# Kernel tuning notes

Hardware: AMD Instinct MI355X
Metric: run time of the kernel (lower is better)

## Reference

```python
import jax, jax.numpy as jnp
import numpy as np

L, B, S, H = 2, 32, 2048, 256  # layers, batch, seqlen, hidden (=input_size)


def setup_inputs() -> dict:
    key = jax.random.key(0)
    k0, k1, k2, k3, k4 = jax.random.split(key, 5)
    scale = 1.0 / np.sqrt(H)
    inputs = jax.random.normal(k0, (B, S, H), jnp.float32)
    W_ih = jax.random.uniform(k1, (L, 4 * H, H), jnp.float32, -scale, scale)
    b_ih = jax.random.uniform(k2, (L, 4 * H), jnp.float32, -scale, scale)
    W_hh = jax.random.uniform(k3, (L, 4 * H, H), jnp.float32, -scale, scale)
    b_hh = jax.random.uniform(k4, (L, 4 * H), jnp.float32, -scale, scale)
    return {"inputs": inputs, "W_ih": W_ih, "b_ih": b_ih, "W_hh": W_hh, "b_hh": b_hh}


def _lstm_layer(x, Wi, bi, Wh, bh):
    # Precompute input projection for the whole sequence (matches cells[l].ih(prev_layer)).
    xp = jnp.einsum('bsh,gh->bsg', x, Wi) + bi  # [B, S, 4H]
    hid = Wh.shape[1]
    h0 = jnp.zeros((x.shape[0], hid), x.dtype)
    c0 = jnp.zeros((x.shape[0], hid), x.dtype)

    def step(carry, xt):
        h, c = carry
        gates = xt + h @ Wh.T + bh          # [B, 4H]
        i, f, g, o = jnp.split(gates, 4, axis=-1)
        c = jax.nn.sigmoid(f) * c + jax.nn.sigmoid(i) * jnp.tanh(g)
        h = jax.nn.sigmoid(o) * jnpp_tanh(c) if False else jax.nn.sigmoid(o) * jnp.tanh(c)
        return (h, c), h

    (hT, cT), ys = jax.lax.scan(step, (h0, c0), jnp.swapaxes(xp, 0, 1))  # scan over time
    return jnp.swapaxes(ys, 0, 1), hT, cT  # [B, S, H], [B, H], [B, H]


def reference(inputs, W_ih, b_ih, W_hh, b_hh):
    # Eval-mode forward: locked dropout is identity; hiddens initialized to zeros.
    x = inputs
    hs, cs = [], []
    for l in range(W_ih.shape[0]):
        x, hT, cT = _lstm_layer(x, W_ih[l], b_ih[l], W_hh[l], b_hh[l])
        hs.append(hT)
        cs.append(cT)
    # outputs [B,S,H]; final hiddens each [L,B,H]
    return x, jnp.stack(hs, axis=0), jnp.stack(cs, axis=0)
```

## Files before the change

### kernel.cpp

```cpp
#include <hip/hip_runtime.h>
#include <cstdint>
#include <cstddef>

typedef _Float16 half_t;
typedef _Float16 half2_t __attribute__((ext_vector_type(2)));
typedef _Float16 half8_t __attribute__((ext_vector_type(8)));
typedef float   float4_t __attribute__((ext_vector_type(4)));

#define L_N 2
#define B_N 32
#define S_N 2048
#define H_N 256
#define G_N 1024
#define M_N (B_N*S_N)

#define RING_R 4
#define RING_BYTES (B_N*RING_R*128*8)

#define WS_A0   0ull
#define WS_XP   33554432ull
#define WS_WI   167772160ull
#define WS_WH   168820736ull
#define WS_BSUM 169869312ull
#define WS_HP0  169877504ull
#define WS_HP1  170008576ull

__global__ void cvt_f32_f16(const float* __restrict__ in, half_t* __restrict__ out, int n){
  int i = blockIdx.x*256 + threadIdx.x;
  if (i < n) out[i] = (half_t)in[i];
}

__global__ void make_bsum(const float* __restrict__ bi, const float* __restrict__ bh,
                          float* __restrict__ bs, int n){
  int i = blockIdx.x*256 + threadIdx.x;
  if (i < n) bs[i] = bi[i] + bh[i];
}

__global__ __launch_bounds__(256) void gemm_xp(
    const half_t* __restrict__ A, const half_t* __restrict__ W,
    const float* __restrict__ bsum, half_t* __restrict__ XP)
{
  const int wave = threadIdx.x >> 6;
  const int lane = threadIdx.x & 63;
  const int l15 = lane & 15, quad = lane >> 4;
  const int m0 = blockIdx.x*64 + wave*16;
  const int n0 = blockIdx.y*64;
  float4_t acc[4] = {{0,0,0,0},{0,0,0,0},{0,0,0,0},{0,0,0,0}};
  const half_t* arow = A + (size_t)(m0 + l15)*H_N + quad*8;
  const half_t* brow[4];
  #pragma unroll
  for (int nt=0; nt<4; ++nt)
    brow[nt] = W + (size_t)(n0 + nt*16 + l15)*H_N + quad*8;
  #pragma unroll
  for (int k0=0; k0<H_N; k0+=32){
    half8_t af = *(const half8_t*)(arow + k0);
    #pragma unroll
    for (int nt=0; nt<4; ++nt){
      half8_t bf = *(const half8_t*)(brow[nt] + k0);
      acc[nt] = __builtin_amdgcn_mfma_f32_16x16x32_f16(af, bf, acc[nt], 0, 0, 0);
    }
  }
  #pragma unroll
  for (int nt=0; nt<4; ++nt){
    const int col = n0 + nt*16 + l15;
    const int cell = col & 255, gate = col >> 8;
    const float bs = bsum[col];
    #pragma unroll
    for (int r=0; r<4; ++r){
      XP[(size_t)(m0 + quad*4 + r)*G_N + cell*4 + gate] = (half_t)(acc[nt][r] + bs);
    }
  }
}

__device__ __forceinline__ float sigf(float x){ return 1.f/(1.f + __expf(-x)); }
__device__ __forceinline__ float tanh_f(float x){ return 1.f - 2.f/(__expf(2.f*x) + 1.f); }

__device__ __forceinline__ uint32_t ring_poll(const unsigned long long* p, unsigned tag){
  unsigned long long v;
  do { v = __hip_atomic_load(p, __ATOMIC_RELAXED, __HIP_MEMORY_SCOPE_AGENT); }
  while ((unsigned)(v >> 32) != tag);
  return (uint32_t)v;
}

__device__ __forceinline__ void wg_barrier_lds(){
  asm volatile("s_waitcnt lgkmcnt(0)" ::: "memory");
  __builtin_amdgcn_s_barrier();
  asm volatile("" ::: "memory");
}

__global__ __launch_bounds__(768) void lstm_fused(
    const uint32_t* __restrict__ Wh0,
    const uint32_t* __restrict__ Wh1,
    const uint32_t* __restrict__ Wi1,
    const half_t*  __restrict__ xp,
    const float*   __restrict__ bsum1,
    unsigned long long* __restrict__ hp0,
    unsigned long long* __restrict__ hp1,
    float* __restrict__ out,
    float* __restrict__ hT, float* __restrict__ cT)
{
  __shared__ __align__(16) uint32_t h0s[128];
  __shared__ __align__(16) uint32_t h1s[128];
  __shared__ float red[6][128];
  const int tid = threadIdx.x;
  const int part = tid >> 7;
  const int r    = tid & 127;
  const int kh   = part & 1;
  const int b  = blockIdx.x & 31;
  const int s  = blockIdx.x >> 5;
  const int g  = r >> 5;
  const int cl = r & 31;
  const int cell = s*32 + cl;

  const uint32_t* wbase =
      (part < 2 ? Wh0 : (part < 4 ? Wh1 : Wi1)) + (size_t)(g*256 + cell)*128 + kh*64;
  uint32_t w[64];
  #pragma unroll
  for (int i=0;i<64;++i) w[i] = wbase[i];

  float bb0=0.f, bb1=0.f, bb2=0.f, bb3=0.f;
  if (tid >= 64 && tid < 96){
    const int mc = s*32 + (tid - 64);
    bb0 = bsum1[      mc];
    bb1 = bsum1[256 + mc];
    bb2 = bsum1[512 + mc];
    bb3 = bsum1[768 + mc];
  }

  unsigned long long* r0 = hp0 + (size_t)b*(RING_R*128);
  unsigned long long* r1 = hp1 + (size_t)b*(RING_R*128);
  const size_t base = (size_t)b * S_N;
  float cst = 0.f;

  for (int t=0; t<=S_N; ++t){
    uint2 xv = {0u,0u};
    if (tid < 32 && t < S_N)
      xv = *(const uint2*)(xp + (base + t)*G_N + (size_t)(s*32 + tid)*4);
    if (tid < 128){
      uint32_t hv = 0u;
      if (t > 0) hv = ring_poll(r0 + (size_t)((t-1)&(RING_R-1))*128 + tid, (unsigned)t);
      h0s[tid] = hv;
    } else if (tid < 256){
      const int j = tid - 128;
      uint32_t hv = 0u;
      if (t > 1) hv = ring_poll(r1 + (size_t)((t-2)&(RING_R-1))*128 + j, (unsigned)(t-1));
      h1s[j] = hv;
    }
    wg_barrier_lds();

    const bool active = (part < 2) ? (t < S_N) : (t >= 1);
    if (active){
      const uint32_t* hsrc = (part == 2 || part == 3) ? h1s : h0s;
      const uint4* h4 = (const uint4*)(hsrc + kh*64);
      float a0=0.f,a1=0.f,a2=0.f,a3=0.f;
      #pragma unroll
      for (int i=0;i<16;++i){
        const uint4 hh = h4[i];
        a0 = __builtin_amdgcn_fdot2(__builtin_bit_cast(half2_t, w[4*i+0]), __builtin_bit_cast(half2_t, hh.x), a0, false);
        a1 = __builtin_amdgcn_fdot2(__builtin_bit_cast(half2_t, w[4*i+1]), __builtin_bit_cast(half2_t, hh.y), a1, false);
        a2 = __builtin_amdgcn_fdot2(__builtin_bit_cast(half2_t, w[4*i+2]), __builtin_bit_cast(half2_t, hh.z), a2, false);
        a3 = __builtin_amdgcn_fdot2(__builtin_bit_cast(half2_t, w[4*i+3]), __builtin_bit_cast(half2_t, hh.w), a3, false);
      }
      red[part][r] = (a0+a1)+(a2+a3);
    }
    wg_barrier_lds();

    if (tid < 32){
      if (t < S_N){
        const int l = tid;
        const half2_t xlo = __builtin_bit_cast(half2_t, xv.x);
        const half2_t xhi = __builtin_bit_cast(half2_t, xv.y);
        const float s0 = red[0][     l] + red[1][     l] + (float)xlo.x;
        const float s1 = red[0][32 + l] + red[1][32 + l] + (float)xlo.y;
        const float s2 = red[0][64 + l] + red[1][64 + l] + (float)xhi.x;
        const float s3 = red[0][96 + l] + red[1][96 + l] + (float)xhi.y;
        const float gi = sigf(s0);
        const float gf = sigf(s1);
        const float gg = tanh_f(s2);
        const float go = sigf(s3);
        cst = gf*cst + gi*gg;
        const float h = go * tanh_f(cst);
        const half_t hv16 = (half_t)h;
        const int hu = (int)__builtin_bit_cast(unsigned short, hv16);
        const int plo = __shfl(hu, 2*l,   64);
        const int phi = __shfl(hu, 2*l+1, 64);
        if (l < 16){
          const unsigned long long val =
              ((unsigned long long)(unsigned)(t+1) << 32)
            | (unsigned long long)((((unsigned)phi & 0xffffu) << 16) | ((unsigned)plo & 0xffffu));
          __hip_atomic_store(r0 + (size_t)(t&(RING_R-1))*128 + s*16 + l, val,
                             __ATOMIC_RELAXED, __HIP_MEMORY_SCOPE_AGENT);
        }
        if (t == S_N-1){ hT[b*H_N + s*32 + l] = h; cT[b*H_N + s*32 + l] = cst; }
      }
    }
    else if (tid >= 64 && tid < 96){
      if (t >= 1){
        const int l = tid - 64;
        const int mc = s*32 + l;
        const float s0 = red[2][     l] + red[3][     l] + red[4][     l] + red[5][     l] + bb0;
        const float s1 = red[2][32 + l] + red[3][32 + l] + red[4][32 + l] + red[5][32 + l] + bb1;
        const float s2 = red[2][64 + l] + red[3][64 + l] + red[4][64 + l] + red[5][64 + l] + bb2;
        const float s3 = red[2][96 + l] + red[3][96 + l] + red[4][96 + l] + red[5][96 + l] + bb3;
        const float gi = sigf(s0);
        const float gf = sigf(s1);
        const float gg = tanh_f(s2);
        const float go = sigf(s3);
        cst = gf*cst + gi*gg;
        const float h = go * tanh_f(cst);
        const half_t hv16 = (half_t)h;
        const int hu = (int)__builtin_bit_cast(unsigned short, hv16);
        const int plo = __shfl(hu, 2*l,   64);
        const int phi = __shfl(hu, 2*l+1, 64);
        if (l < 16){
          const unsigned long long val =
              ((unsigned long long)(unsigned)t << 32)
            | (unsigned long long)((((unsigned)phi & 0xffffu) << 16) | ((unsigned)plo & 0xffffu));
          __hip_atomic_store(r1 + (size_t)((t-1)&(RING_R-1))*128 + s*16 + l, val,
                             __ATOMIC_RELAXED, __HIP_MEMORY_SCOPE_AGENT);
        }
        out[(base + (t-1))*H_N + mc] = h;
        if (t == S_N){ hT[B_N*H_N + b*H_N + mc] = h; cT[B_N*H_N + b*H_N + mc] = cst; }
      }
    }
  }
}

extern "C" void kernel_launch(void* const* d_in, const int* in_sizes, int n_in,
                              void* d_out, int out_size, void* d_ws, size_t ws_size,
                              hipStream_t stream)
{
  const float* x   = (const float*)d_in[0];
  const float* Wih = (const float*)d_in[1];
  const float* bih = (const float*)d_in[2];
  const float* Whh = (const float*)d_in[3];
  const float* bhh = (const float*)d_in[4];
  float* out = (float*)d_out;

  char* ws = (char*)d_ws;
  half_t* A0   = (half_t*)(ws + WS_A0);
  half_t* XP   = (half_t*)(ws + WS_XP);
  half_t* Wi16 = (half_t*)(ws + WS_WI);
  half_t* Wh16 = (half_t*)(ws + WS_WH);
  float*  bsum = (float*)(ws + WS_BSUM);
  unsigned long long* hp0 = (unsigned long long*)(ws + WS_HP0);
  unsigned long long* hp1 = (unsigned long long*)(ws + WS_HP1);

  cvt_f32_f16<<<dim3(M_N*H_N/256), dim3(256), 0, stream>>>(x, A0, M_N*H_N);
  cvt_f32_f16<<<dim3(L_N*G_N*H_N/256), dim3(256), 0, stream>>>(Wih, Wi16, L_N*G_N*H_N);
  cvt_f32_f16<<<dim3(L_N*G_N*H_N/256), dim3(256), 0, stream>>>(Whh, Wh16, L_N*G_N*H_N);
  make_bsum<<<dim3(L_N*G_N/256), dim3(256), 0, stream>>>(bih, bhh, bsum, L_N*G_N);

  float* hT = out + (size_t)M_N*H_N;
  float* cT = hT + (size_t)L_N*B_N*H_N;

  gemm_xp<<<dim3(M_N/64, G_N/64), dim3(256), 0, stream>>>(A0, Wi16, bsum, XP);

  hipMemsetAsync(hp0, 0, 2*RING_BYTES, stream);

  lstm_fused<<<dim3(B_N*8), dim3(768), 0, stream>>>(
      (const uint32_t*)Wh16,
      (const uint32_t*)(Wh16 + (size_t)G_N*H_N),
      (const uint32_t*)(Wi16 + (size_t)G_N*H_N),
      XP, bsum + G_N, hp0, hp1, out, hT, cT);
}
```

Before: 3.955 ms.

## Poll h-exchange ring via fast cache-level loads with periodic system-coherent fallback

Replaces the agent-scope atomic polling of the cross-block hidden-state ring with inline-asm loads using sc0 (a nearer cache level), falling back every eighth iteration to a fully coherent sc0 sc1 load. Each publish now writes to two mirror rings, one with a plain store and one with a coherent store. An epoch counter bumped per launch is folded into the tags so stale values from earlier launches cannot match. The aim is to cut the per-timestep spin latency between dependent blocks. The risk is extra store traffic and correctness that relies on cache-coherence behaviour across CUs.

```diff
diff --git a/kernel.cpp b/kernel.cpp
--- a/kernel.cpp
+++ b/kernel.cpp
@@ -17,13 +17,16 @@
 #define RING_R 4
 #define RING_BYTES (B_N*RING_R*128*8)
 
-#define WS_A0   0ull
-#define WS_XP   33554432ull
-#define WS_WI   167772160ull
-#define WS_WH   168820736ull
-#define WS_BSUM 169869312ull
-#define WS_HP0  169877504ull
-#define WS_HP1  170008576ull
+#define WS_A0    0ull
+#define WS_XP    33554432ull
+#define WS_WI    167772160ull
+#define WS_WH    168820736ull
+#define WS_BSUM  169869312ull
+#define WS_HP0   169877504ull
+#define WS_HP1   170008576ull
+#define WS_HPF0  170139648ull
+#define WS_HPF1  170270720ull
+#define WS_EPOCH 170401792ull
 
 __global__ void cvt_f32_f16(const float* __restrict__ in, half_t* __restrict__ out, int n){
   int i = blockIdx.x*256 + threadIdx.x;
@@ -35,6 +38,8 @@
   int i = blockIdx.x*256 + threadIdx.x;
   if (i < n) bs[i] = bi[i] + bh[i];
 }
+
+__global__ void bump_epoch(unsigned* e){ if (threadIdx.x == 0) *e = *e + 1u; }
 
 __global__ __launch_bounds__(256) void gemm_xp(
     const half_t* __restrict__ A, const half_t* __restrict__ W,
@@ -75,11 +80,31 @@
 __device__ __forceinline__ float sigf(float x){ return 1.f/(1.f + __expf(-x)); }
 __device__ __forceinline__ float tanh_f(float x){ return 1.f - 2.f/(__expf(2.f*x) + 1.f); }
 
-__device__ __forceinline__ uint32_t ring_poll(const unsigned long long* p, unsigned tag){
+__device__ __forceinline__ uint32_t ring_poll2(const unsigned long long* pf,
+                                               const unsigned long long* ps,
+                                               unsigned tag){
   unsigned long long v;
-  do { v = __hip_atomic_load(p, __ATOMIC_RELAXED, __HIP_MEMORY_SCOPE_AGENT); }
-  while ((unsigned)(v >> 32) != tag);
-  return (uint32_t)v;
+  int k = 0;
+  for (;;){
+    asm volatile("global_load_dwordx2 %0, %1, off sc0\n\t"
+                 "s_waitcnt vmcnt(0)"
+                 : "=&v"(v) : "v"(pf) : "memory");
+    if ((unsigned)(v >> 32) == tag) return (uint32_t)v;
+    if ((++k & 7) == 0){
+      asm volatile("global_load_dwordx2 %0, %1, off sc0 sc1\n\t"
+                   "s_waitcnt vmcnt(0)"
+                   : "=&v"(v) : "v"(ps) : "memory");
+      if ((unsigned)(v >> 32) == tag) return (uint32_t)v;
+    }
+  }
+}
+
+__device__ __forceinline__ void ring_publish(unsigned long long* pf,
+                                             unsigned long long* ps,
+                                             unsigned long long val){
+  asm volatile("global_store_dwordx2 %0, %2, off\n\t"
+               "global_store_dwordx2 %1, %2, off sc0 sc1"
+               :: "v"(pf), "v"(ps), "v"(val) : "memory");
 }
 
 __device__ __forceinline__ void wg_barrier_lds(){
@@ -96,6 +121,9 @@
     const float*   __restrict__ bsum1,
     unsigned long long* __restrict__ hp0,
     unsigned long long* __restrict__ hp1,
+    unsigned long long* __restrict__ hf0,
+    unsigned long long* __restrict__ hf1,
+    const unsigned* __restrict__ ep,
     float* __restrict__ out,
     float* __restrict__ hT, float* __restrict__ cT)
 {
@@ -112,6 +140,9 @@
   const int cl = r & 31;
   const int cell = s*32 + cl;
 
+  const unsigned epoch = __hip_atomic_load(ep, __ATOMIC_RELAXED, __HIP_MEMORY_SCOPE_AGENT);
+  const unsigned tbase = ((epoch & 0x7FFFFu) + 1u) << 12;
+
   const uint32_t* wbase =
       (part < 2 ? Wh0 : (part < 4 ? Wh1 : Wi1)) + (size_t)(g*256 + cell)*128 + kh*64;
   uint32_t w[64];
@@ -129,6 +160,8 @@
 
   unsigned long long* r0 = hp0 + (size_t)b*(RING_R*128);
   unsigned long long* r1 = hp1 + (size_t)b*(RING_R*128);
+  unsigned long long* f0 = hf0 + (size_t)b*(RING_R*128);
+  unsigned long long* f1 = hf1 + (size_t)b*(RING_R*128);
   const size_t base = (size_t)b * S_N;
   float cst = 0.f;
 
@@ -138,12 +171,18 @@
       xv = *(const uint2*)(xp + (base + t)*G_N + (size_t)(s*32 + tid)*4);
     if (tid < 128){
       uint32_t hv = 0u;
-      if (t > 0) hv = ring_poll(r0 + (size_t)((t-1)&(RING_R-1))*128 + tid, (unsigned)t);
+      if (t > 0){
+        const size_t o = (size_t)((t-1)&(RING_R-1))*128 + tid;
+        hv = ring_poll2(f0 + o, r0 + o, tbase + (unsigned)t);
+      }
       h0s[tid] = hv;
     } else if (tid < 256){
       const int j = tid - 128;
       uint32_t hv = 0u;
-      if (t > 1) hv = ring_poll(r1 + (size_t)((t-2)&(RING_R-1))*128 + j, (unsigned)(t-1));
+      if (t > 1){
+        const size_t o = (size_t)((t-2)&(RING_R-1))*128 + j;
+        hv = ring_poll2(f1 + o, r1 + o, tbase + (unsigned)(t-1));
+      }
       h1s[j] = hv;
     }
     wg_barrier_lds();
@@ -186,10 +225,10 @@
         const int phi = __shfl(hu, 2*l+1, 64);
         if (l < 16){
           const unsigned long long val =
-              ((unsigned long long)(unsigned)(t+1) << 32)
+              ((unsigned long long)(tbase + (unsigned)(t+1)) << 32)
             | (unsigned long long)((((unsigned)phi & 0xffffu) << 16) | ((unsigned)plo & 0xffffu));
-          __hip_atomic_store(r0 + (size_t)(t&(RING_R-1))*128 + s*16 + l, val,
-                             __ATOMIC_RELAXED, __HIP_MEMORY_SCOPE_AGENT);
+          const size_t o = (size_t)(t&(RING_R-1))*128 + s*16 + l;
+          ring_publish(f0 + o, r0 + o, val);
         }
         if (t == S_N-1){ hT[b*H_N + s*32 + l] = h; cT[b*H_N + s*32 + l] = cst; }
       }
@@ -214,10 +253,10 @@
         const int phi = __shfl(hu, 2*l+1, 64);
         if (l < 16){
           const unsigned long long val =
-              ((unsigned long long)(unsigned)t << 32)
+              ((unsigned long long)(tbase + (unsigned)t) << 32)
             | (unsigned long long)((((unsigned)phi & 0xffffu) << 16) | ((unsigned)plo & 0xffffu));
-          __hip_atomic_store(r1 + (size_t)((t-1)&(RING_R-1))*128 + s*16 + l, val,
-                             __ATOMIC_RELAXED, __HIP_MEMORY_SCOPE_AGENT);
+          const size_t o = (size_t)((t-1)&(RING_R-1))*128 + s*16 + l;
+          ring_publish(f1 + o, r1 + o, val);
         }
         out[(base + (t-1))*H_N + mc] = h;
         if (t == S_N){ hT[B_N*H_N + b*H_N + mc] = h; cT[B_N*H_N + b*H_N + mc] = cst; }
@@ -245,22 +284,26 @@
   float*  bsum = (float*)(ws + WS_BSUM);
   unsigned long long* hp0 = (unsigned long long*)(ws + WS_HP0);
   unsigned long long* hp1 = (unsigned long long*)(ws + WS_HP1);
+  unsigned long long* hf0 = (unsigned long long*)(ws + WS_HPF0);
+  unsigned long long* hf1 = (unsigned long long*)(ws + WS_HPF1);
+  unsigned* ep = (unsigned*)(ws + WS_EPOCH);
 
   cvt_f32_f16<<<dim3(M_N*H_N/256), dim3(256), 0, stream>>>(x, A0, M_N*H_N);
   cvt_f32_f16<<<dim3(L_N*G_N*H_N/256), dim3(256), 0, stream>>>(Wih, Wi16, L_N*G_N*H_N);
   cvt_f32_f16<<<dim3(L_N*G_N*H_N/256), dim3(256), 0, stream>>>(Whh, Wh16, L_N*G_N*H_N);
   make_bsum<<<dim3(L_N*G_N/256), dim3(256), 0, stream>>>(bih, bhh, bsum, L_N*G_N);
+  bump_epoch<<<dim3(1), dim3(64), 0, stream>>>(ep);
 
   float* hT = out + (size_t)M_N*H_N;
   float* cT = hT + (size_t)L_N*B_N*H_N;
 
   gemm_xp<<<dim3(M_N/64, G_N/64), dim3(256), 0, stream>>>(A0, Wi16, bsum, XP);
 
-  hipMemsetAsync(hp0, 0, 2*RING_BYTES, stream);
+  hipMemsetAsync(hp0, 0, 4*RING_BYTES, stream);
 
   lstm_fused<<<dim3(B_N*8), dim3(768), 0, stream>>>(
       (const uint32_t*)Wh16,
       (const uint32_t*)(Wh16 + (size_t)G_N*H_N),
       (const uint32_t*)(Wi16 + (size_t)G_N*H_N),
-      XP, bsum + G_N, hp0, hp1, out, hT, cT);
-}
+      XP, bsum + G_N, hp0, hp1, hf0, hf1, ep, out, hT, cT);
+}
```

Measured after the change: 6.498 ms. 64.3% more time.
